# Kernel tuning notes

Measured on AMD Instinct MI355X. Metric: run time of the kernel, lower is better.

Reference implementation:

```python
import jax, jax.numpy as jnp
import numpy as np

HIDDEN = 64
SEQ_LEN = 128
BATCH = 64
T_MAX = 20.0
BW = 1.0


def setup_inputs() -> dict:
    key = jax.random.key(0)
    ks = jax.random.split(key, 8)
    s = 1.0 / np.sqrt(HIDDEN)
    return {
        "rand_uniform_pool": jax.random.uniform(ks[0], (BATCH, SEQ_LEN), jnp.float32, 1e-6, 1.0),
        "expert_time": jax.random.uniform(ks[1], (BATCH, SEQ_LEN), jnp.float32, 0.0, 1.0),
        "W_ih": jax.random.uniform(ks[2], (4 * HIDDEN, 1), jnp.float32, -s, s),
        "W_hh": jax.random.uniform(ks[3], (4 * HIDDEN, HIDDEN), jnp.float32, -s, s),
        "b_ih": jax.random.uniform(ks[4], (4 * HIDDEN,), jnp.float32, -s, s),
        "b_hh": jax.random.uniform(ks[5], (4 * HIDDEN,), jnp.float32, -s, s),
        "V_w": jax.random.uniform(ks[6], (1, HIDDEN), jnp.float32, -s, s),
        "V_b": jax.random.uniform(ks[7], (1,), jnp.float32, -s, s),
    }


def _generate_time(rand_uniform_pool, W_ih, W_hh, b_ih, b_hh, V_w, V_b):
    # sequential rollout over SEQ_LEN steps (data-dependent recurrence)
    u_seq = rand_uniform_pool.T[:, :, None]  # [S, B, 1]

    def step(carry, u):
        hx, cx, cum = carry
        sigma = jax.nn.elu(hx @ V_w.T + V_b) + 1.0            # [B, 1]
        cum = cum + (-jnp.log(u)) / sigma                      # exponential inter-event time
        gates = cum @ W_ih.T + b_ih + hx @ W_hh.T + b_hh       # [B, 4H]
        i, f, g, o = jnp.split(gates, 4, axis=1)               # torch LSTMCell gate order
        cx = jax.nn.sigmoid(f) * cx + jax.nn.sigmoid(i) * jnp.tanh(g)
        hx = jax.nn.sigmoid(o) * jnp.tanh(cx)
        return (hx, cx, cum), cum[:, 0]

    init = (jnp.zeros((BATCH, HIDDEN), jnp.float32),
            jnp.zeros((BATCH, HIDDEN), jnp.float32),
            jnp.zeros((BATCH, 1), jnp.float32))
    _, cums = jax.lax.scan(step, init, u_seq)                  # [S, B]
    return cums.T                                              # [B, S]


def _reward(expert_time, learner_time):
    N = BATCH * SEQ_LEN
    t_l = learner_time.reshape(N)
    t_e = expert_time.reshape(N)
    m_l = ((t_l < T_MAX) & (t_l > 0)).astype(jnp.float32)
    m_e = ((t_e < T_MAX) & (t_e > 0)).astype(jnp.float32)

    def ksum(a, b, ma, mb):
        # ma^T exp(-(a-b)^2/bw) mb without storing more than one NxN matrix at a time
        K = jnp.exp(-((b[:, None] - a[None, :]) ** 2) / BW)    # [N, N]
        return jnp.dot(mb, K @ ma)

    ee = ksum(t_e, t_e, m_e, m_e)
    ll = ksum(t_l, t_l, m_l, m_l)
    le = ksum(t_l, t_e, m_l, m_e)
    return (ee + ll - 2.0 * le).reshape(1, 1)


def reference(rand_uniform_pool, expert_time, W_ih, W_hh, b_ih, b_hh, V_w, V_b):
    learner_time = _generate_time(rand_uniform_pool, W_ih, W_hh, b_ih, b_hh, V_w, V_b)
    loss = _reward(expert_time, learner_time)
    return loss
```

## Files before the change

kernel.cpp:

```cpp
#include <hip/hip_runtime.h>
#include <math.h>

#define HIDDEN 64
#define SEQ 128
#define BATCH 64
#define NPTS (BATCH * SEQ)
#define TMAXV 20.0f
#define L2E 1.4426950408889634f
#define LN2 0.6931471805599453f

typedef float v2f __attribute__((ext_vector_type(2)));

__device__ __forceinline__ float fexp2(float x) { return __builtin_amdgcn_exp2f(x); }
__device__ __forceinline__ float flog2(float x) { return __builtin_amdgcn_logf(x); }
__device__ __forceinline__ float frcp(float x)  { return __builtin_amdgcn_rcpf(x); }
__device__ __forceinline__ float fsigmoid(float x) { return frcp(1.0f + fexp2(-x * L2E)); }
__device__ __forceinline__ float ftanh(float x)    { return 1.0f - 2.0f * frcp(1.0f + fexp2(2.0f * x * L2E)); }

__device__ __forceinline__ void barrier_lds_only() {
    asm volatile("s_waitcnt lgkmcnt(0)" ::: "memory");
    __builtin_amdgcn_s_barrier();
}

template <int CTRL>
__device__ __forceinline__ float dpp_mov(float x) {
    int r = __builtin_amdgcn_update_dpp(0, __float_as_int(x), CTRL, 0xf, 0xf, false);
    return __int_as_float(r);
}
__device__ __forceinline__ float wave_sum_dpp(float x) {
    x += dpp_mov<0x111>(x);
    x += dpp_mov<0x112>(x);
    x += dpp_mov<0x114>(x);
    x += dpp_mov<0x118>(x);
    x += dpp_mov<0x142>(x);
    x += dpp_mov<0x143>(x);
    return __int_as_float(__builtin_amdgcn_readlane(__float_as_int(x), 63));
}

__device__ __forceinline__ float wave_sum_shfl(float v) {
    v += __shfl_xor(v, 1);  v += __shfl_xor(v, 2);  v += __shfl_xor(v, 4);
    v += __shfl_xor(v, 8);  v += __shfl_xor(v, 16); v += __shfl_xor(v, 32);
    return v;
}

__global__ __launch_bounds__(256) void gen_and_ee(
    const float* __restrict__ upool,
    const float* __restrict__ texp,
    const float* __restrict__ Wih,
    const float* __restrict__ Whh,
    const float* __restrict__ bih,
    const float* __restrict__ bhh,
    const float* __restrict__ Vw,
    const float* __restrict__ Vb,
    float* __restrict__ tl,
    float* __restrict__ out)
{
    __shared__ __align__(16) float w_s[16][256][4];
    __shared__ float lu_s[SEQ];
    __shared__ float act_s[2][256];
    __shared__ __align__(16) float hx_s[4][64];
    __shared__ float2 qbuf[2048];

    const int bid = blockIdx.x;
    const int tid = threadIdx.x;

    if (bid < BATCH) {
        const int h  = tid & 63;
        const int wv = tid >> 6;

        {
            const float4* wrow = (const float4*)(Whh + tid * 64);
            float4* wdst = (float4*)w_s;
            #pragma unroll
            for (int k = 0; k < 16; ++k) wdst[k * 256 + tid] = wrow[k];
        }
        const float bias = bih[tid] + bhh[tid];
        const float wih  = Wih[tid];
        const float vw   = Vw[h];
        const float vb   = Vb[0];

        if (tid < SEQ) lu_s[tid] = -flog2(upool[bid * SEQ + tid]) * LN2;
        hx_s[wv][h] = 0.0f;
        float cx = 0.0f;
        barrier_lds_only();

        float sg0 = (vb > 0.0f) ? (vb + 1.0f) : fexp2(vb * L2E);
        float cum = lu_s[0] * frcp(sg0);
        float keep = (tid == 0) ? cum : 0.0f;

        const float4* wl = ((const float4*)w_s) + tid;

        #pragma unroll 1
        for (int s = 0; s < SEQ - 1; ++s) {
            const float4* h4 = (const float4*)hx_s[wv];
            v2f a0 = {0.f, 0.f}, a1 = {0.f, 0.f}, a2 = {0.f, 0.f}, a3 = {0.f, 0.f};
            #pragma unroll
            for (int k = 0; k < 16; k += 2) {
                float4 wA = wl[k * 256];
                float4 wB = wl[(k + 1) * 256];
                float4 va = h4[k];
                float4 vbq = h4[k + 1];
                a0 = a0 + (v2f){wA.x, wA.y} * (v2f){va.x, va.y};
                a1 = a1 + (v2f){wA.z, wA.w} * (v2f){va.z, va.w};
                a2 = a2 + (v2f){wB.x, wB.y} * (v2f){vbq.x, vbq.y};
                a3 = a3 + (v2f){wB.z, wB.w} * (v2f){vbq.z, vbq.w};
            }
            v2f aa = (a0 + a1) + (a2 + a3);
            float g = (aa.x + aa.y) + bias + cum * wih;
            float a = (wv == 2) ? ftanh(g) : fsigmoid(g);
            act_s[s & 1][tid] = a;
            barrier_lds_only();

            float ig = act_s[s & 1][h];
            float fg = act_s[s & 1][64 + h];
            float gg = act_s[s & 1][128 + h];
            float og = act_s[s & 1][192 + h];
            cx = fg * cx + ig * gg;
            float hx = og * ftanh(cx);
            hx_s[wv][h] = hx;

            float tot = wave_sum_dpp(hx * vw);
            float xx  = tot + vb;
            float sg  = (xx > 0.0f) ? (xx + 1.0f) : fexp2(xx * L2E);
            cum += lu_s[s + 1] * frcp(sg);

            keep = (tid == s + 1) ? cum : keep;
        }
        if (tid < SEQ) tl[bid * SEQ + tid] = keep;
    } else {
        const int eb = bid - BATCH;
        const int pc = eb & 31;
        const int qs = eb >> 5;

        const int p = pc * 256 + tid;
        const float tp = texp[p];
        const float mp = (tp < TMAXV && tp > 0.0f) ? 1.0f : 0.0f;

        const int q0 = qs * 2048;
        for (int i = tid; i < 2048; i += 256) {
            float tq = texp[q0 + i];
            float mq = (tq < TMAXV && tq > 0.0f) ? 1.0f : 0.0f;
            qbuf[i] = make_float2(tq, mq);
        }
        __syncthreads();

        float acc = 0.0f;
        #pragma unroll 4
        for (int i = 0; i < 2048; ++i) {
            float2 qq = qbuf[i];
            float d = tp - qq.x;
            acc = fmaf(qq.y, fexp2(d * d * (-L2E)), acc);
        }
        acc *= mp;
        acc = wave_sum_shfl(acc);
        if ((tid & 63) == 0) atomicAdd(out, acc);
    }
}

__global__ __launch_bounds__(256) void ll_le(
    const float* __restrict__ texp,
    const float* __restrict__ tl,
    float* __restrict__ out)
{
    __shared__ __align__(16) float4 qbuf[512];
    __shared__ float red[4];

    const int pc = blockIdx.x;
    const int qs = blockIdx.y;
    const int tid = threadIdx.x;

    const int p = pc * 256 + tid;
    const float tlp = tl[p];
    const float mlp = (tlp < TMAXV && tlp > 0.0f) ? 1.0f : 0.0f;

    const int q0 = qs * 512;
    for (int i = tid; i < 512; i += 256) {
        float tq = tl[q0 + i];
        float mq = (tq < TMAXV && tq > 0.0f) ? 1.0f : 0.0f;
        float te = texp[q0 + i];
        float me = (te < TMAXV && te > 0.0f) ? 1.0f : 0.0f;
        qbuf[i] = make_float4(tq, mq, te, me);
    }
    __syncthreads();

    float val = 0.0f;
    if (__ballot(mlp != 0.0f) != 0ULL) {
        float a_ll = 0.0f, a_le = 0.0f;
        #pragma unroll 4
        for (int i = 0; i < 512; ++i) {
            float4 q = qbuf[i];
            float d1 = tlp - q.x;
            a_ll = fmaf(q.y, fexp2(d1 * d1 * (-L2E)), a_ll);
            float d2 = tlp - q.z;
            a_le = fmaf(q.w, fexp2(d2 * d2 * (-L2E)), a_le);
        }
        val = mlp * (a_ll - 2.0f * a_le);
    }

    val = wave_sum_shfl(val);
    if ((tid & 63) == 0) red[tid >> 6] = val;
    __syncthreads();
    if (tid == 0) atomicAdd(out, red[0] + red[1] + red[2] + red[3]);
}

extern "C" void kernel_launch(void* const* d_in, const int* in_sizes, int n_in,
                              void* d_out, int out_size, void* d_ws, size_t ws_size,
                              hipStream_t stream) {
    const float* upool = (const float*)d_in[0];
    const float* texp  = (const float*)d_in[1];
    const float* Wih   = (const float*)d_in[2];
    const float* Whh   = (const float*)d_in[3];
    const float* bih   = (const float*)d_in[4];
    const float* bhh   = (const float*)d_in[5];
    const float* Vw    = (const float*)d_in[6];
    const float* Vb    = (const float*)d_in[7];
    float* out = (float*)d_out;
    float* tl  = (float*)d_ws;

    hipMemsetAsync(out, 0, sizeof(float), stream);
    hipLaunchKernelGGL(gen_and_ee, dim3(BATCH + 128), dim3(256), 0, stream,
                       upool, texp, Wih, Whh, bih, bhh, Vw, Vb, tl, out);
    hipLaunchKernelGGL(ll_le, dim3(32, 16), dim3(256), 0, stream, texp, tl, out);
}
```

Measured before the change: 167.6 us.

## Hold LSTM recurrent weights in registers using 512-thread blocks with paired-lane dot products

The recurrent W_hh matrix now lives in registers instead of LDS. Each gate row is split across two lanes that each keep 32 weights, and the partial sums are combined with a DPP xor-1 swap. This removes the per-step LDS weight reads from the serial LSTM rollout. Blocks grow to 512 threads, and the ee-kernel blocks are reshaped to cover 512 points so the grid shrinks accordingly. In exchange there is higher register pressure and fewer ee blocks, which means less parallelism for that part.

```diff
diff --git a/kernel.cpp b/kernel.cpp
--- a/kernel.cpp
+++ b/kernel.cpp
@@ -26,6 +26,9 @@
 __device__ __forceinline__ float dpp_mov(float x) {
     int r = __builtin_amdgcn_update_dpp(0, __float_as_int(x), CTRL, 0xf, 0xf, false);
     return __int_as_float(r);
+}
+__device__ __forceinline__ v2f dpp_xor1_v2(v2f v) {
+    v2f r; r.x = dpp_mov<0xB1>(v.x); r.y = dpp_mov<0xB1>(v.y); return r;
 }
 __device__ __forceinline__ float wave_sum_dpp(float x) {
     x += dpp_mov<0x111>(x);
@@ -43,7 +46,7 @@
     return v;
 }
 
-__global__ __launch_bounds__(256) void gen_and_ee(
+__global__ __launch_bounds__(512, 1) void gen_and_ee(
     const float* __restrict__ upool,
     const float* __restrict__ texp,
     const float* __restrict__ Wih,
@@ -55,32 +58,56 @@
     float* __restrict__ tl,
     float* __restrict__ out)
 {
-    __shared__ __align__(16) float w_s[16][256][4];
-    __shared__ float lu_s[SEQ];
-    __shared__ float act_s[2][256];
-    __shared__ __align__(16) float hx_s[4][64];
-    __shared__ float2 qbuf[2048];
+    __shared__ __align__(16) float smem[17056];
 
     const int bid = blockIdx.x;
     const int tid = threadIdx.x;
 
     if (bid < BATCH) {
-        const int h  = tid & 63;
+        const int r  = tid >> 1;
+        const int p  = tid & 1;
+        const int l  = tid & 63;
         const int wv = tid >> 6;
 
+        float* stage = smem + tid * 32;
+        float* act   = smem;
+        float* hxw   = smem + 16384 + wv * 64;
+        float* lu_s  = smem + 16896;
+
         {
-            const float4* wrow = (const float4*)(Whh + tid * 64);
-            float4* wdst = (float4*)w_s;
+            const float* wrow = Whh + r * 64;
             #pragma unroll
-            for (int k = 0; k < 16; ++k) wdst[k * 256 + tid] = wrow[k];
-        }
-        const float bias = bih[tid] + bhh[tid];
-        const float wih  = Wih[tid];
-        const float vw   = Vw[h];
+            for (int k = 0; k < 8; ++k) {
+                float2 lo = *(const float2*)(wrow + 8 * k + 2 * p);
+                float2 hi = *(const float2*)(wrow + 8 * k + 4 + 2 * p);
+                *(float2*)(stage + 2 * k)      = lo;
+                *(float2*)(stage + 16 + 2 * k) = hi;
+            }
+        }
+        __syncthreads();
+
+        v2f wlo[8], whi[8];
+        {
+            const float4* s4 = (const float4*)stage;
+            #pragma unroll
+            for (int m = 0; m < 4; ++m) {
+                float4 a = s4[m];
+                float4 b = s4[4 + m];
+                wlo[2 * m]     = (v2f){a.x, a.y};
+                wlo[2 * m + 1] = (v2f){a.z, a.w};
+                whi[2 * m]     = (v2f){b.x, b.y};
+                whi[2 * m + 1] = (v2f){b.z, b.w};
+            }
+        }
+
+        const float bias = bih[r] + bhh[r];
+        const float wih  = Wih[r];
+        const float vwl  = Vw[l];
         const float vb   = Vb[0];
+        const int   gsel = r >> 6;
 
         if (tid < SEQ) lu_s[tid] = -flog2(upool[bid * SEQ + tid]) * LN2;
-        hx_s[wv][h] = 0.0f;
+        hxw[l] = 0.0f;
         float cx = 0.0f;
         barrier_lds_only();
 
@@ -88,38 +115,34 @@
         float cum = lu_s[0] * frcp(sg0);
         float keep = (tid == 0) ? cum : 0.0f;
 
-        const float4* wl = ((const float4*)w_s) + tid;
-
         #pragma unroll 1
         for (int s = 0; s < SEQ - 1; ++s) {
-            const float4* h4 = (const float4*)hx_s[wv];
-            v2f a0 = {0.f, 0.f}, a1 = {0.f, 0.f}, a2 = {0.f, 0.f}, a3 = {0.f, 0.f};
+            const v2f* h2 = (const v2f*)hxw;
+            v2f alo = {0.f, 0.f}, ahi = {0.f, 0.f};
             #pragma unroll
-            for (int k = 0; k < 16; k += 2) {
-                float4 wA = wl[k * 256];
-                float4 wB = wl[(k + 1) * 256];
-                float4 va = h4[k];
-                float4 vbq = h4[k + 1];
-                a0 = a0 + (v2f){wA.x, wA.y} * (v2f){va.x, va.y};
-                a1 = a1 + (v2f){wA.z, wA.w} * (v2f){va.z, va.w};
-                a2 = a2 + (v2f){wB.x, wB.y} * (v2f){vbq.x, vbq.y};
-                a3 = a3 + (v2f){wB.z, wB.w} * (v2f){vbq.z, vbq.w};
+            for (int k = 0; k < 8; ++k) {
+                v2f hlo = h2[4 * k + p];
+                v2f hhi = h2[4 * k + 2 + p];
+                alo += wlo[k] * hlo;
+                ahi += whi[k] * hhi;
             }
-            v2f aa = (a0 + a1) + (a2 + a3);
+            v2f slo = alo + dpp_xor1_v2(alo);
+            v2f shi = ahi + dpp_xor1_v2(ahi);
+            v2f aa  = slo + shi;
             float g = (aa.x + aa.y) + bias + cum * wih;
-            float a = (wv == 2) ? ftanh(g) : fsigmoid(g);
-            act_s[s & 1][tid] = a;
+            float a = (gsel == 2) ? ftanh(g) : fsigmoid(g);
+            if (p == 0) act[(s & 1) * 256 + r] = a;
             barrier_lds_only();
 
-            float ig = act_s[s & 1][h];
-            float fg = act_s[s & 1][64 + h];
-            float gg = act_s[s & 1][128 + h];
-            float og = act_s[s & 1][192 + h];
+            float ig = act[(s & 1) * 256 + l];
+            float fg = act[(s & 1) * 256 + 64 + l];
+            float gg = act[(s & 1) * 256 + 128 + l];
+            float og = act[(s & 1) * 256 + 192 + l];
             cx = fg * cx + ig * gg;
             float hx = og * ftanh(cx);
-            hx_s[wv][h] = hx;
-
-            float tot = wave_sum_dpp(hx * vw);
+            hxw[l] = hx;
+
+            float tot = wave_sum_dpp(hx * vwl);
             float xx  = tot + vb;
             float sg  = (xx > 0.0f) ? (xx + 1.0f) : fexp2(xx * L2E);
             cum += lu_s[s + 1] * frcp(sg);
@@ -129,15 +152,17 @@
         if (tid < SEQ) tl[bid * SEQ + tid] = keep;
     } else {
         const int eb = bid - BATCH;
-        const int pc = eb & 31;
-        const int qs = eb >> 5;
-
-        const int p = pc * 256 + tid;
-        const float tp = texp[p];
+        const int pc = eb & 15;
+        const int qs = eb >> 4;
+
+        float2* qbuf = (float2*)smem;
+
+        const int pp = pc * 512 + tid;
+        const float tp = texp[pp];
         const float mp = (tp < TMAXV && tp > 0.0f) ? 1.0f : 0.0f;
 
         const int q0 = qs * 2048;
-        for (int i = tid; i < 2048; i += 256) {
+        for (int i = tid; i < 2048; i += 512) {
             float tq = texp[q0 + i];
             float mq = (tq < TMAXV && tq > 0.0f) ? 1.0f : 0.0f;
             qbuf[i] = make_float2(tq, mq);
@@ -218,7 +243,7 @@
     float* tl  = (float*)d_ws;
 
     hipMemsetAsync(out, 0, sizeof(float), stream);
-    hipLaunchKernelGGL(gen_and_ee, dim3(BATCH + 128), dim3(256), 0, stream,
+    hipLaunchKernelGGL(gen_and_ee, dim3(BATCH + 64), dim3(512), 0, stream,
                        upool, texp, Wih, Whh, bih, bhh, Vw, Vb, tl, out);
     hipLaunchKernelGGL(ll_le, dim3(32, 16), dim3(256), 0, stream, texp, tl, out);
 }
```

Measured after the change: 168.3 us. No clear change (+0.4%).
